# Kernel optimization log

Hardware: AMD Instinct MI355X
Metric: run time of the kernel (lower is better)

Reference implementation:

```python
import jax, jax.numpy as jnp
import numpy as np

B, T, D = 8, 1024, 1024
H = 16
ATT_DIM = 1024
VAL_DIM = 1024
SCALE = float((D // H) ** 0.5)  # note: uses input_dim//num_heads, not head dim of attention_dim
EPS = 1e-13


def setup_inputs() -> dict:
    key = jax.random.key(0)
    ks = jax.random.split(key, 6)
    inputs = jax.random.normal(ks[0], (B, T, D), dtype=jnp.float32)
    mask = jnp.ones((B, T), dtype=jnp.float32)
    adj = jax.random.uniform(ks[1], (B, T, T), dtype=jnp.float32)
    # combined QKV projection: Linear(D, 2*ATT_DIM + VAL_DIM)
    W_qkv = jax.random.normal(ks[2], (2 * ATT_DIM + VAL_DIM, D), dtype=jnp.float32) * (1.0 / np.sqrt(D))
    b_qkv = jnp.zeros((2 * ATT_DIM + VAL_DIM,), dtype=jnp.float32)
    # output projection: Linear(VAL_DIM, D)
    W_out = jax.random.normal(ks[3], (D, VAL_DIM), dtype=jnp.float32) * (1.0 / np.sqrt(VAL_DIM))
    b_out = jnp.zeros((D,), dtype=jnp.float32)
    return {"inputs": inputs, "mask": mask, "adj": adj,
            "W_qkv": W_qkv, "b_qkv": b_qkv, "W_out": W_out, "b_out": b_out}


def reference(inputs, mask, adj, W_qkv, b_qkv, W_out, b_out):
    b, t, _ = inputs.shape
    dh_a = ATT_DIM // H
    dh_v = VAL_DIM // H
    proj = jnp.einsum('btd,od->bto', inputs, W_qkv) + b_qkv
    q = proj[..., :ATT_DIM]
    k = proj[..., ATT_DIM:2 * ATT_DIM]
    v = proj[..., 2 * ATT_DIM:]
    # [B, H, T, dh]
    q = q.reshape(b, t, H, dh_a).transpose(0, 2, 1, 3)
    k = k.reshape(b, t, H, dh_a).transpose(0, 2, 1, 3)
    v = v.reshape(b, t, H, dh_v).transpose(0, 2, 1, 3)
    scores = jnp.einsum('bhqd,bhkd->bhqk', q, k) / SCALE
    # multiplicative adjacency gate, broadcast over heads
    scores = scores * adj[:, None, :, :]
    # old-allennlp masked_softmax: softmax(scores * mask), re-mask, renormalize
    m = mask[:, None, None, :]  # [B,1,1,T]
    attn = jax.nn.softmax(scores * m, axis=-1)
    attn = attn * m
    attn = attn / (attn.sum(axis=-1, keepdims=True) + EPS)
    out = jnp.einsum('bhqk,bhkd->bhqd', attn, v)  # [B,H,T,dh_v]
    out = out.transpose(0, 2, 1, 3).reshape(b, t, VAL_DIM)
    out = jnp.einsum('btv,ov->bto', out, W_out) + b_out
    return out
```

## Files before the change

### kernel.cpp

```cpp
#include <hip/hip_runtime.h>
#include <hip/hip_bf16.h>
#include <cstdint>


using bf16 = __hip_bfloat16;
typedef __attribute__((ext_vector_type(8))) short short8;
typedef __attribute__((ext_vector_type(4))) short short4v;
typedef __attribute__((ext_vector_type(4))) float floatx4;
typedef __attribute__((ext_vector_type(2))) unsigned int uint2v;

#define B_    8
#define T_    1024
#define D_    1024
#define H_    16
#define PROJW 3072

__device__ __forceinline__ void gl2lds16(const void* g, void* l) {
  __builtin_amdgcn_global_load_lds(
      (const __attribute__((address_space(1))) void*)g,
      (__attribute__((address_space(3))) void*)l,
      16, 0, 0);
}

__device__ __forceinline__ unsigned short f2b_bits(float f) {
  return __builtin_bit_cast(unsigned short, __float2bfloat16(f));
}

__device__ __forceinline__ short8 pack8(floatx4 a, floatx4 b) {
  short8 h;
  h[0] = f2b_bits(a[0]); h[1] = f2b_bits(a[1]);
  h[2] = f2b_bits(a[2]); h[3] = f2b_bits(a[3]);
  h[4] = f2b_bits(b[0]); h[5] = f2b_bits(b[1]);
  h[6] = f2b_bits(b[2]); h[7] = f2b_bits(b[3]);
  return h;
}

__device__ __forceinline__ float fast_exp2(float x) {
#if __has_builtin(__builtin_amdgcn_exp2f)
  return __builtin_amdgcn_exp2f(x);
#else
  float r;
  asm("v_exp_f32 %0, %1\ns_nop 0" : "=v"(r) : "v"(x));
  return r;
#endif
}

__global__ __launch_bounds__(512)
void gemm_qkv_f32(const float* __restrict__ A, const float* __restrict__ Bw,
                  const float* __restrict__ bias, bf16* __restrict__ Qp,
                  bf16* __restrict__ Kp, bf16* __restrict__ Vt,
                  int M, int N, int K)
{
  __shared__ __align__(16) unsigned short sA[2][128 * 64];
  __shared__ __align__(16) unsigned short sB[2][128 * 64];

  const int tid  = threadIdx.x;
  const int lane = tid & 63;
  const int wv   = tid >> 6;
  const int quad = lane >> 4;
  const int l16  = lane & 15;
  const int wm   = wv >> 1;
  const int wn   = wv & 1;

  const int gx   = gridDim.x;
  const int nwg  = gx * gridDim.y;
  const int bidl = blockIdx.y * gx + blockIdx.x;
  const int xcd  = bidl & 7;
  const int c    = bidl >> 3;
  const int cpx  = nwg >> 3;
  const int R    = cpx / gx;
  const int nb   = c / (R * 4);
  const int rem  = c % (R * 4);
  const int bm   = xcd * R + (rem >> 2);
  const int bn   = nb * 4 + (rem & 3);

  floatx4 acc[2][4];
#pragma unroll
  for (int i = 0; i < 2; ++i)
#pragma unroll
    for (int j = 0; j < 4; ++j) acc[i][j] = (floatx4){0.f, 0.f, 0.f, 0.f};

  const int o_base = wv * 1024 + lane * 16;
  const float* gAf[2];
  const float* gBf[2];
  int ldsOff[2];
#pragma unroll
  for (int it = 0; it < 2; ++it) {
    int o   = it * 8192 + o_base;
    int row = o >> 7;
    int col = ((o & 127) ^ ((row & 7) << 4)) >> 1;
    gAf[it] = A  + (size_t)(bm * 128 + row) * K + col;
    gBf[it] = Bw + (size_t)(bn * 128 + row) * K + col;
    ldsOff[it] = ((it * 8192 + wv * 1024) >> 1) + lane * 8;
  }

  const int NT = K >> 6;

  {
    floatx4 a0a = *(const floatx4*)(gAf[0]);
    floatx4 a0b = *(const floatx4*)(gAf[0] + 4);
    floatx4 a1a = *(const floatx4*)(gAf[1]);
    floatx4 a1b = *(const floatx4*)(gAf[1] + 4);
    floatx4 b0a = *(const floatx4*)(gBf[0]);
    floatx4 b0b = *(const floatx4*)(gBf[0] + 4);
    floatx4 b1a = *(const floatx4*)(gBf[1]);
    floatx4 b1b = *(const floatx4*)(gBf[1] + 4);
    *(short8*)&sA[0][ldsOff[0]] = pack8(a0a, a0b);
    *(short8*)&sA[0][ldsOff[1]] = pack8(a1a, a1b);
    *(short8*)&sB[0][ldsOff[0]] = pack8(b0a, b0b);
    *(short8*)&sB[0][ldsOff[1]] = pack8(b1a, b1b);
    asm volatile("s_waitcnt lgkmcnt(0)" ::: "memory");
    __builtin_amdgcn_s_barrier();
  }

  const int swx = (l16 & 7) << 3;

  for (int t = 0; t < NT; ++t) {
    const int s = t & 1;
    floatx4 a0a, a0b, a1a, a1b, b0a, b0b, b1a, b1b;
    if (t + 1 < NT) {
      const size_t ko = (size_t)(t + 1) * 64;
      a0a = *(const floatx4*)(gAf[0] + ko);
      a0b = *(const floatx4*)(gAf[0] + ko + 4);
      a1a = *(const floatx4*)(gAf[1] + ko);
      a1b = *(const floatx4*)(gAf[1] + ko + 4);
      b0a = *(const floatx4*)(gBf[0] + ko);
      b0b = *(const floatx4*)(gBf[0] + ko + 4);
      b1a = *(const floatx4*)(gBf[1] + ko);
      b1b = *(const floatx4*)(gBf[1] + ko + 4);
    }
    __builtin_amdgcn_sched_barrier(0);

#pragma unroll
    for (int kk = 0; kk < 64; kk += 32) {
      short8 a_[2], b_[4];
#pragma unroll
      for (int i = 0; i < 2; ++i)
        a_[i] = *(const short8*)&sA[s][(wm * 32 + i * 16 + l16) * 64 + ((kk + quad * 8) ^ swx)];
#pragma unroll
      for (int j = 0; j < 4; ++j)
        b_[j] = *(const short8*)&sB[s][(wn * 64 + j * 16 + l16) * 64 + ((kk + quad * 8) ^ swx)];
#pragma unroll
      for (int i = 0; i < 2; ++i)
#pragma unroll
        for (int j = 0; j < 4; ++j)
          acc[i][j] = __builtin_amdgcn_mfma_f32_16x16x32_bf16(a_[i], b_[j], acc[i][j], 0, 0, 0);
    }

    __builtin_amdgcn_sched_barrier(0);
    if (t + 1 < NT) {
      asm volatile("s_waitcnt vmcnt(0)" ::: "memory");
      *(short8*)&sA[s ^ 1][ldsOff[0]] = pack8(a0a, a0b);
      *(short8*)&sA[s ^ 1][ldsOff[1]] = pack8(a1a, a1b);
      *(short8*)&sB[s ^ 1][ldsOff[0]] = pack8(b0a, b0b);
      *(short8*)&sB[s ^ 1][ldsOff[1]] = pack8(b1a, b1b);
      asm volatile("s_waitcnt lgkmcnt(0)" ::: "memory");
    }
    __builtin_amdgcn_sched_barrier(0);
    __builtin_amdgcn_s_barrier();
  }

  {
    const int region = bn >> 3;
    if (region < 2) {
      bf16* dst = region == 0 ? Qp : Kp;
#pragma unroll
      for (int j = 0; j < 4; ++j) {
        const int colg = bn * 128 + wn * 64 + j * 16 + l16;
        const int colr = colg & 1023;
        const float bv = bias[colg];
#pragma unroll
        for (int i = 0; i < 2; ++i)
#pragma unroll
          for (int r = 0; r < 4; ++r) {
            int rowg = bm * 128 + wm * 32 + i * 16 + quad * 4 + r;
            dst[(size_t)rowg * 1024 + colr] = __float2bfloat16(acc[i][j][r] + bv);
          }
      }
    } else {
#pragma unroll
      for (int j = 0; j < 4; ++j) {
        const int colg = bn * 128 + wn * 64 + j * 16 + l16;
        const int d  = colg & 63;
        const int hh = (colg >> 6) & 15;
        const float bv = bias[colg];
#pragma unroll
        for (int i = 0; i < 2; ++i) {
          int rowg0 = bm * 128 + wm * 32 + i * 16 + quad * 4;
          int bb = rowg0 >> 10, t0 = rowg0 & 1023;
          short4v pk;
#pragma unroll
          for (int r = 0; r < 4; ++r) pk[r] = (short)f2b_bits(acc[i][j][r] + bv);
          *(short4v*)&Vt[((size_t)(bb * 16 + hh) << 16) + ((size_t)d << 10) + t0] = pk;
        }
      }
    }
  }
}

__global__ __launch_bounds__(512)
void gemm_out_f32b(const bf16* __restrict__ A, const float* __restrict__ Bw,
                   const float* __restrict__ bias, float* __restrict__ C0,
                   int M, int N, int K)
{
  __shared__ __align__(16) unsigned short sA[2][128 * 64];
  __shared__ __align__(16) unsigned short sB[2][128 * 64];

  const int tid  = threadIdx.x;
  const int lane = tid & 63;
  const int wv   = tid >> 6;
  const int quad = lane >> 4;
  const int l16  = lane & 15;
  const int wm   = wv >> 1;
  const int wn   = wv & 1;

  const int gx   = gridDim.x;
  const int nwg  = gx * gridDim.y;
  const int bidl = blockIdx.y * gx + blockIdx.x;
  const int xcd  = bidl & 7;
  const int c    = bidl >> 3;
  const int cpx  = nwg >> 3;
  const int R    = cpx / gx;
  const int nb   = c / (R * 4);
  const int rem  = c % (R * 4);
  const int bm   = xcd * R + (rem >> 2);
  const int bn   = nb * 4 + (rem & 3);

  floatx4 acc[2][4];
#pragma unroll
  for (int i = 0; i < 2; ++i)
#pragma unroll
    for (int j = 0; j < 4; ++j) acc[i][j] = (floatx4){0.f, 0.f, 0.f, 0.f};

  const int o_base = wv * 1024 + lane * 16;
  const bf16*  gA[2];
  const float* gBf[2];
  int ldsOff[2];
#pragma unroll
  for (int it = 0; it < 2; ++it) {
    int o   = it * 8192 + o_base;
    int row = o >> 7;
    int col = ((o & 127) ^ ((row & 7) << 4)) >> 1;
    gA[it]  = A  + (size_t)(bm * 128 + row) * K + col;
    gBf[it] = Bw + (size_t)(bn * 128 + row) * K + col;
    ldsOff[it] = ((it * 8192 + wv * 1024) >> 1) + lane * 8;
  }

  const int NT = K >> 6;

  {
    floatx4 q0a = *(const floatx4*)(gBf[0]);
    floatx4 q0b = *(const floatx4*)(gBf[0] + 4);
    floatx4 q1a = *(const floatx4*)(gBf[1]);
    floatx4 q1b = *(const floatx4*)(gBf[1] + 4);
#pragma unroll
    for (int it = 0; it < 2; ++it)
      gl2lds16(gA[it], &sA[0][(it * 8192 + wv * 1024) >> 1]);
    *(short8*)&sB[0][ldsOff[0]] = pack8(q0a, q0b);
    *(short8*)&sB[0][ldsOff[1]] = pack8(q1a, q1b);
    asm volatile("s_waitcnt lgkmcnt(0)" ::: "memory");
  }

  const int swx = (l16 & 7) << 3;

  for (int t = 0; t < NT; ++t) {
    const int s = t & 1;
    floatx4 q0a, q0b, q1a, q1b;
    if (t + 1 < NT) {
      q0a = *(const floatx4*)(gBf[0] + (size_t)(t + 1) * 64);
      q0b = *(const floatx4*)(gBf[0] + (size_t)(t + 1) * 64 + 4);
      q1a = *(const floatx4*)(gBf[1] + (size_t)(t + 1) * 64);
      q1b = *(const floatx4*)(gBf[1] + (size_t)(t + 1) * 64 + 4);
#pragma unroll
      for (int it = 0; it < 2; ++it)
        gl2lds16(gA[it] + (size_t)(t + 1) * 64, &sA[s ^ 1][(it * 8192 + wv * 1024) >> 1]);
      __builtin_amdgcn_sched_barrier(0);
      asm volatile("s_waitcnt vmcnt(6)" ::: "memory");
    } else {
      asm volatile("s_waitcnt vmcnt(0)" ::: "memory");
    }
    __builtin_amdgcn_s_barrier();
    __builtin_amdgcn_sched_barrier(0);

#pragma unroll
    for (int kk = 0; kk < 64; kk += 32) {
      short8 a_[2], b_[4];
#pragma unroll
      for (int i = 0; i < 2; ++i)
        a_[i] = *(const short8*)&sA[s][(wm * 32 + i * 16 + l16) * 64 + ((kk + quad * 8) ^ swx)];
#pragma unroll
      for (int j = 0; j < 4; ++j)
        b_[j] = *(const short8*)&sB[s][(wn * 64 + j * 16 + l16) * 64 + ((kk + quad * 8) ^ swx)];
#pragma unroll
      for (int i = 0; i < 2; ++i)
#pragma unroll
        for (int j = 0; j < 4; ++j)
          acc[i][j] = __builtin_amdgcn_mfma_f32_16x16x32_bf16(a_[i], b_[j], acc[i][j], 0, 0, 0);
    }

    __builtin_amdgcn_sched_barrier(0);
    if (t + 1 < NT) {
      asm volatile("s_waitcnt vmcnt(2)" ::: "memory");
      *(short8*)&sB[s ^ 1][ldsOff[0]] = pack8(q0a, q0b);
      *(short8*)&sB[s ^ 1][ldsOff[1]] = pack8(q1a, q1b);
      asm volatile("s_waitcnt lgkmcnt(0)" ::: "memory");
    }
    __builtin_amdgcn_sched_barrier(0);
    __builtin_amdgcn_s_barrier();
  }

#pragma unroll
  for (int j = 0; j < 4; ++j) {
    const int colg = bn * 128 + wn * 64 + j * 16 + l16;
    const float bv = bias[colg];
#pragma unroll
    for (int i = 0; i < 2; ++i)
#pragma unroll
      for (int r = 0; r < 4; ++r) {
        int rowg = bm * 128 + wm * 32 + i * 16 + quad * 4 + r;
        C0[(size_t)rowg * N + colg] = acc[i][j][r] + bv;
      }
  }
}

__global__ __launch_bounds__(512)
void attn_fused(const bf16* __restrict__ Qp, const bf16* __restrict__ Kp,
                const bf16* __restrict__ Vt, const float* __restrict__ adj,
                const float* __restrict__ mask, bf16* __restrict__ aout)
{
  __shared__ __align__(16) unsigned short sK[64 * 72];
  __shared__ __align__(16) unsigned short sVT[64 * 72];
  __shared__ __align__(16) unsigned short sP[128 * 72];

  const int tid  = threadIdx.x;
  const int lane = tid & 63;
  const int wv   = tid >> 6;
  const int quad = lane >> 4;
  const int l16  = lane & 15;

  const int bid  = blockIdx.x + 16 * (blockIdx.y + 8 * blockIdx.z);
  const int b    = bid & 7;
  const int slot = bid >> 3;
  const int h    = slot & 15;
  const int qt   = slot >> 4;

  const bf16* qbase = Qp + (size_t)(b * T_ + qt * 128 + wv * 16 + l16) * 1024 + h * 64 + quad * 8;
  const short8 aq0 = *(const short8*)qbase;
  const short8 aq1 = *(const short8*)(qbase + 32);

  const int srow  = tid >> 3;
  const int chunk = (tid & 7) * 8;
  const int sig = ((srow & 15) << 2) | (srow >> 4);
  const bf16* kb = Kp + (size_t)(b * T_ + sig) * 1024 + h * 64 + chunk;
  const bf16* vb = Vt + ((size_t)(b * 16 + h) << 16) + ((size_t)srow << 10) + chunk;

  const float* mb = mask + b * T_ + l16 * 4;
  const float* adjr[4];
#pragma unroll
  for (int r = 0; r < 4; ++r)
    adjr[r] = adj + ((size_t)b * T_ + qt * 128 + wv * 16 + quad * 4 + r) * T_ + l16 * 4;

  short8 kr = *(const short8*)kb;
  short8 vr = *(const short8*)vb;

  short8 ones8;
#pragma unroll
  for (int i = 0; i < 8; ++i) ones8[i] = (short)0x3F80;

  floatx4 oacc[4];
#pragma unroll
  for (int d = 0; d < 4; ++d) oacc[d] = (floatx4){0.f, 0.f, 0.f, 0.f};
  floatx4 Lacc = (floatx4){0.f, 0.f, 0.f, 0.f};

  const float SC = 0.125f * 1.44269504088896f;

  for (int kt = 0; kt < 16; ++kt) {
    floatx4 av[4];
    floatx4 mk4 = *(const floatx4*)(mb + kt * 64);
#pragma unroll
    for (int r = 0; r < 4; ++r) av[r] = *(const floatx4*)(adjr[r] + kt * 64);
    floatx4 cjv, offv;
#pragma unroll
    for (int j = 0; j < 4; ++j) {
      cjv[j]  = mk4[j] * SC;
      offv[j] = (mk4[j] == 0.f) ? -1e30f : 0.f;
    }

    __syncthreads();
    *(short8*)&sK [srow * 72 + chunk] = kr;
    *(short8*)&sVT[srow * 72 + chunk] = vr;
    __syncthreads();

    {
      int nk = kt < 15 ? kt + 1 : 15;
      kr = *(const short8*)(kb + ((size_t)nk << 16));
      vr = *(const short8*)(vb + (nk << 6));
    }

    floatx4 sacc[4];
#pragma unroll
    for (int j = 0; j < 4; ++j) sacc[j] = (floatx4){0.f, 0.f, 0.f, 0.f};
    __builtin_amdgcn_s_setprio(1);
#pragma unroll
    for (int kk = 0; kk < 64; kk += 32) {
      short8 aq = kk ? aq1 : aq0;
#pragma unroll
      for (int j = 0; j < 4; ++j) {
        short8 bk = *(const short8*)&sK[(j * 16 + l16) * 72 + kk + quad * 8];
        sacc[j] = __builtin_amdgcn_mfma_f32_16x16x32_bf16(aq, bk, sacc[j], 0, 0, 0);
      }
    }
    __builtin_amdgcn_s_setprio(0);

#pragma unroll
    for (int r = 0; r < 4; ++r) {
      floatx4 avc = av[r] * cjv;
      float p[4];
#pragma unroll
      for (int j = 0; j < 4; ++j) {
        float z = fminf(fmaf(sacc[j][r], avc[j], offv[j]), 100.f);
        p[j] = fast_exp2(z);
      }
      unsigned w0, w1;
      asm("v_cvt_pk_bf16_f32 %0, %1, %2" : "=v"(w0) : "v"(p[0]), "v"(p[1]));
      asm("v_cvt_pk_bf16_f32 %0, %1, %2" : "=v"(w1) : "v"(p[2]), "v"(p[3]));
      uint2v pw; pw[0] = w0; pw[1] = w1;
      *(uint2v*)&sP[(wv * 16 + quad * 4 + r) * 72 + l16 * 4] = pw;
    }

    __asm__ __volatile__("" ::: "memory");

    __builtin_amdgcn_s_setprio(1);
#pragma unroll
    for (int kk = 0; kk < 64; kk += 32) {
      short8 ap = *(const short8*)&sP[(wv * 16 + l16) * 72 + kk + quad * 8];
      Lacc = __builtin_amdgcn_mfma_f32_16x16x32_bf16(ap, ones8, Lacc, 0, 0, 0);
#pragma unroll
      for (int d = 0; d < 4; ++d) {
        short8 bv = *(const short8*)&sVT[(d * 16 + l16) * 72 + kk + quad * 8];
        oacc[d] = __builtin_amdgcn_mfma_f32_16x16x32_bf16(ap, bv, oacc[d], 0, 0, 0);
      }
    }
    __builtin_amdgcn_s_setprio(0);
  }

#pragma unroll
  for (int d = 0; d < 4; ++d) {
#pragma unroll
    for (int r = 0; r < 4; ++r) {
      int qrow = qt * 128 + wv * 16 + quad * 4 + r;
      float val = oacc[d][r] / (Lacc[r] + 1e-13f);
      aout[(size_t)(b * T_ + qrow) * 1024 + h * 64 + d * 16 + l16] = __float2bfloat16(val);
    }
  }
}

extern "C" void kernel_launch(void* const* d_in, const int* in_sizes, int n_in,
                              void* d_out, int out_size, void* d_ws, size_t ws_size,
                              hipStream_t stream) {
  const float* inputs = (const float*)d_in[0];
  const float* mask   = (const float*)d_in[1];
  const float* adj    = (const float*)d_in[2];
  const float* W_qkv  = (const float*)d_in[3];
  const float* b_qkv  = (const float*)d_in[4];
  const float* W_out  = (const float*)d_in[5];
  const float* b_out  = (const float*)d_in[6];

  const size_t SEG = (size_t)8192 * 1024;
  bf16* Qp   = (bf16*)d_ws;
  bf16* Kp   = Qp + SEG;
  bf16* Vt   = Kp + SEG;
  bf16* aout = Vt + SEG;

  gemm_qkv_f32<<<dim3(PROJW / 128, (B_ * T_) / 128), dim3(512), 0, stream>>>(
      inputs, W_qkv, b_qkv, Qp, Kp, Vt, B_ * T_, PROJW, D_);
  attn_fused<<<dim3(H_, T_ / 128, B_), dim3(512), 0, stream>>>(Qp, Kp, Vt, adj, mask, aout);
  gemm_out_f32b<<<dim3(D_ / 128, (B_ * T_) / 128), dim3(512), 0, stream>>>(
      aout, W_out, b_out, (float*)d_out, B_ * T_, D_, D_);
}
```

Measured before the change: 301.0 us.

## Pre-convert QKV GEMM input to bf16 and stream A tiles directly into LDS

Adds a separate kernel that converts the fp32 input activations to bf16, using the output buffer as scratch. The QKV GEMM then loads its A operand with global_load_lds straight into shared memory, while the fp32 weights are still converted in registers. The K-loop's waits and barriers are reworked so the next tile's async loads overlap the current MFMA work. This halves the A-operand read traffic per tile and removes its per-element packing inside the GEMM, at the cost of an extra pass over the input and an extra kernel launch.

```diff
diff --git a/kernel.cpp b/kernel.cpp
--- a/kernel.cpp
+++ b/kernel.cpp
@@ -45,11 +45,23 @@
 #endif
 }
 
+__global__ __launch_bounds__(256)
+void cvt_f32_bf16(const float* __restrict__ src, bf16* __restrict__ dst, int n) {
+  int i = (blockIdx.x * 256 + threadIdx.x) * 4;
+  if (i < n) {
+    floatx4 f = *(const floatx4*)(src + i);
+    short4v h;
+    h[0] = f2b_bits(f[0]); h[1] = f2b_bits(f[1]);
+    h[2] = f2b_bits(f[2]); h[3] = f2b_bits(f[3]);
+    *(short4v*)(dst + i) = h;
+  }
+}
+
 __global__ __launch_bounds__(512)
-void gemm_qkv_f32(const float* __restrict__ A, const float* __restrict__ Bw,
-                  const float* __restrict__ bias, bf16* __restrict__ Qp,
-                  bf16* __restrict__ Kp, bf16* __restrict__ Vt,
-                  int M, int N, int K)
+void gemm_qkv_f32b(const bf16* __restrict__ A, const float* __restrict__ Bw,
+                   const float* __restrict__ bias, bf16* __restrict__ Qp,
+                   bf16* __restrict__ Kp, bf16* __restrict__ Vt,
+                   int M, int N, int K)
 {
   __shared__ __align__(16) unsigned short sA[2][128 * 64];
   __shared__ __align__(16) unsigned short sB[2][128 * 64];
@@ -81,7 +93,7 @@
     for (int j = 0; j < 4; ++j) acc[i][j] = (floatx4){0.f, 0.f, 0.f, 0.f};
 
   const int o_base = wv * 1024 + lane * 16;
-  const float* gAf[2];
+  const bf16*  gA[2];
   const float* gBf[2];
   int ldsOff[2];
 #pragma unroll
@@ -89,7 +101,7 @@
     int o   = it * 8192 + o_base;
     int row = o >> 7;
     int col = ((o & 127) ^ ((row & 7) << 4)) >> 1;
-    gAf[it] = A  + (size_t)(bm * 128 + row) * K + col;
+    gA[it]  = A  + (size_t)(bm * 128 + row) * K + col;
     gBf[it] = Bw + (size_t)(bn * 128 + row) * K + col;
     ldsOff[it] = ((it * 8192 + wv * 1024) >> 1) + lane * 8;
   }
@@ -97,38 +109,37 @@
   const int NT = K >> 6;
 
   {
-    floatx4 a0a = *(const floatx4*)(gAf[0]);
-    floatx4 a0b = *(const floatx4*)(gAf[0] + 4);
-    floatx4 a1a = *(const floatx4*)(gAf[1]);
-    floatx4 a1b = *(const floatx4*)(gAf[1] + 4);
-    floatx4 b0a = *(const floatx4*)(gBf[0]);
-    floatx4 b0b = *(const floatx4*)(gBf[0] + 4);
-    floatx4 b1a = *(const floatx4*)(gBf[1]);
-    floatx4 b1b = *(const floatx4*)(gBf[1] + 4);
-    *(short8*)&sA[0][ldsOff[0]] = pack8(a0a, a0b);
-    *(short8*)&sA[0][ldsOff[1]] = pack8(a1a, a1b);
-    *(short8*)&sB[0][ldsOff[0]] = pack8(b0a, b0b);
-    *(short8*)&sB[0][ldsOff[1]] = pack8(b1a, b1b);
+    floatx4 q0a = *(const floatx4*)(gBf[0]);
+    floatx4 q0b = *(const floatx4*)(gBf[0] + 4);
+    floatx4 q1a = *(const floatx4*)(gBf[1]);
+    floatx4 q1b = *(const floatx4*)(gBf[1] + 4);
+#pragma unroll
+    for (int it = 0; it < 2; ++it)
+      gl2lds16(gA[it], &sA[0][(it * 8192 + wv * 1024) >> 1]);
+    *(short8*)&sB[0][ldsOff[0]] = pack8(q0a, q0b);
+    *(short8*)&sB[0][ldsOff[1]] = pack8(q1a, q1b);
     asm volatile("s_waitcnt lgkmcnt(0)" ::: "memory");
-    __builtin_amdgcn_s_barrier();
   }
 
   const int swx = (l16 & 7) << 3;
 
   for (int t = 0; t < NT; ++t) {
     const int s = t & 1;
-    floatx4 a0a, a0b, a1a, a1b, b0a, b0b, b1a, b1b;
+    floatx4 q0a, q0b, q1a, q1b;
     if (t + 1 < NT) {
-      const size_t ko = (size_t)(t + 1) * 64;
-      a0a = *(const floatx4*)(gAf[0] + ko);
-      a0b = *(const floatx4*)(gAf[0] + ko + 4);
-      a1a = *(const floatx4*)(gAf[1] + ko);
-      a1b = *(const floatx4*)(gAf[1] + ko + 4);
-      b0a = *(const floatx4*)(gBf[0] + ko);
-      b0b = *(const floatx4*)(gBf[0] + ko + 4);
-      b1a = *(const floatx4*)(gBf[1] + ko);
-      b1b = *(const floatx4*)(gBf[1] + ko + 4);
-    }
+      q0a = *(const floatx4*)(gBf[0] + (size_t)(t + 1) * 64);
+      q0b = *(const floatx4*)(gBf[0] + (size_t)(t + 1) * 64 + 4);
+      q1a = *(const floatx4*)(gBf[1] + (size_t)(t + 1) * 64);
+      q1b = *(const floatx4*)(gBf[1] + (size_t)(t + 1) * 64 + 4);
+#pragma unroll
+      for (int it = 0; it < 2; ++it)
+        gl2lds16(gA[it] + (size_t)(t + 1) * 64, &sA[s ^ 1][(it * 8192 + wv * 1024) >> 1]);
+      __builtin_amdgcn_sched_barrier(0);
+      asm volatile("s_waitcnt vmcnt(6)" ::: "memory");
+    } else {
+      asm volatile("s_waitcnt vmcnt(0)" ::: "memory");
+    }
+    __builtin_amdgcn_s_barrier();
     __builtin_amdgcn_sched_barrier(0);
 
 #pragma unroll
@@ -149,11 +160,9 @@
 
     __builtin_amdgcn_sched_barrier(0);
     if (t + 1 < NT) {
-      asm volatile("s_waitcnt vmcnt(0)" ::: "memory");
-      *(short8*)&sA[s ^ 1][ldsOff[0]] = pack8(a0a, a0b);
-      *(short8*)&sA[s ^ 1][ldsOff[1]] = pack8(a1a, a1b);
-      *(short8*)&sB[s ^ 1][ldsOff[0]] = pack8(b0a, b0b);
-      *(short8*)&sB[s ^ 1][ldsOff[1]] = pack8(b1a, b1b);
+      asm volatile("s_waitcnt vmcnt(2)" ::: "memory");
+      *(short8*)&sB[s ^ 1][ldsOff[0]] = pack8(q0a, q0b);
+      *(short8*)&sB[s ^ 1][ldsOff[1]] = pack8(q1a, q1b);
       asm volatile("s_waitcnt lgkmcnt(0)" ::: "memory");
     }
     __builtin_amdgcn_sched_barrier(0);
@@ -472,8 +481,12 @@
   bf16* Vt   = Kp + SEG;
   bf16* aout = Vt + SEG;
 
-  gemm_qkv_f32<<<dim3(PROJW / 128, (B_ * T_) / 128), dim3(512), 0, stream>>>(
-      inputs, W_qkv, b_qkv, Qp, Kp, Vt, B_ * T_, PROJW, D_);
+  bf16* ib_bf = (bf16*)d_out;
+
+  dim3 blk(256);
+  cvt_f32_bf16<<<dim3(8192 * 1024 / 4 / 256), blk, 0, stream>>>(inputs, ib_bf, 8192 * 1024);
+  gemm_qkv_f32b<<<dim3(PROJW / 128, (B_ * T_) / 128), dim3(512), 0, stream>>>(
+      ib_bf, W_qkv, b_qkv, Qp, Kp, Vt, B_ * T_, PROJW, D_);
   attn_fused<<<dim3(H_, T_ / 128, B_), dim3(512), 0, stream>>>(Qp, Kp, Vt, adj, mask, aout);
   gemm_out_f32b<<<dim3(D_ / 128, (B_ * T_) / 128), dim3(512), 0, stream>>>(
       aout, W_out, b_out, (float*)d_out, B_ * T_, D_, D_);
```

New measurement: 290.3 us. 3.6% less time.
